# Kernel optimization log

Hardware: AMD Instinct MI355X
Metric: run time of the kernel (lower is better)

## Reference

```python
import jax, jax.numpy as jnp
import numpy as np
from functools import partial

THRESH = 0.6      # objectness sigmoid threshold (forward arg `thresh`)
CASE = 416.0      # input image size (forward arg `case`)
NMS_THRESH = 0.7  # nms(boxes, 0.7, mode='inter')
K_PER_SCALE = 512 # fixed candidate cap per scale (jit-safe stand-in for nonzero())
NEG = -1e9


def _decode_scale(out, t, anchors):
    """out: [N, 3*(5+nc), H, W] -> (boxes [K,9], valid [K]) top-K by objectness."""
    N, C, H, W = out.shape
    v = out.transpose(0, 2, 3, 1).reshape(N, H, W, 3, -1)  # [N,H,W,3,5+nc]
    f = v.dtype
    obj = jax.nn.sigmoid(v[..., 0])                        # cfd = sigmoid(vecs[:,0])
    gy = jnp.arange(H, dtype=f).reshape(1, H, 1, 1)        # idxs[:,1] (row)
    gx = jnp.arange(W, dtype=f).reshape(1, 1, W, 1)        # idxs[:,2] (col)
    gn = jnp.arange(N, dtype=f).reshape(N, 1, 1, 1)
    cx = (gx + v[..., 1]) * t / CASE
    cy = (gy + v[..., 2]) * t / CASE
    w = anchors[:, 0] * jnp.exp(v[..., 3]) / CASE          # anchors[a,0], a = last axis
    h = anchors[:, 1] * jnp.exp(v[..., 4]) / CASE
    cls = jnp.argmax(v[..., 5:], axis=-1).astype(f)
    parts = jnp.broadcast_arrays(gn, cx, cy, w, h, obj, cls, gy + 0 * cx, gx + 0 * cx)
    boxes = jnp.stack(parts, axis=-1).reshape(-1, 9)       # [N*H*W*3, 9]
    mask = (obj > THRESH).reshape(-1)
    score = jnp.where(mask, obj.reshape(-1), NEG)
    k = min(K_PER_SCALE, score.shape[0])
    top_s, top_i = jax.lax.top_k(score, k)
    boxes_k = jnp.take(boxes, top_i, axis=0)
    valid_k = top_s > NEG / 2
    if k < K_PER_SCALE:  # pad to fixed K
        pad = K_PER_SCALE - k
        boxes_k = jnp.concatenate([boxes_k, jnp.zeros((pad, 9), f)], 0)
        valid_k = jnp.concatenate([valid_k, jnp.zeros((pad,), bool)], 0)
    return boxes_k, valid_k


def _nms_inter(boxes, valid):
    """Greedy NMS, iou mode 'inter' = inter_area / min(area_i, area_j)."""
    score = jnp.where(valid, boxes[:, 5], NEG)
    order = jnp.argsort(-score)
    boxes = jnp.take(boxes, order, axis=0)
    valid = jnp.take(valid, order)
    cx, cy, w, h = boxes[:, 1], boxes[:, 2], boxes[:, 3], boxes[:, 4]
    x1, y1, x2, y2 = cx - w / 2, cy - h / 2, cx + w / 2, cy + h / 2
    area = jnp.maximum(x2 - x1, 0) * jnp.maximum(y2 - y1, 0)
    ix = jnp.maximum(0.0, jnp.minimum(x2[:, None], x2[None]) - jnp.maximum(x1[:, None], x1[None]))
    iy = jnp.maximum(0.0, jnp.minimum(y2[:, None], y2[None]) - jnp.maximum(y1[:, None], y1[None]))
    inter = ix * iy
    iou = inter / jnp.maximum(jnp.minimum(area[:, None], area[None]), 1e-9)
    M = boxes.shape[0]
    idx = jnp.arange(M)

    def body(i, keep):
        sup = (iou[i] > NMS_THRESH) & keep[i] & (idx > i)
        return keep & ~sup

    keep = jax.lax.fori_loop(0, M, body, valid)
    return boxes * keep[:, None].astype(boxes.dtype)  # suppressed rows zeroed


def reference(out13, out26, out52, anchors13, anchors26, anchors52):
    b13, v13 = _decode_scale(out13, 32.0, anchors13)
    b26, v26 = _decode_scale(out26, 16.0, anchors26)
    b52, v52 = _decode_scale(out52, 8.0, anchors52)
    boxes = jnp.concatenate([b13, b26, b52], axis=0)   # [3K, 9]
    valid = jnp.concatenate([v13, v26, v52], axis=0)
    return _nms_inter(boxes, valid)


def setup_inputs() -> dict:
    key = jax.random.key(0)
    k = jax.random.split(key, 6)
    N, NC = 32, 80
    C = 3 * (5 + NC)
    return {
        "out13": jax.random.normal(k[0], (N, C, 13, 13), jnp.float32),
        "out26": jax.random.normal(k[1], (N, C, 26, 26), jnp.float32),
        "out52": jax.random.normal(k[2], (N, C, 52, 52), jnp.float32),
        "anchors13": jnp.array([[116, 90], [156, 198], [373, 326]], jnp.float32),
        "anchors26": jnp.array([[30, 61], [62, 45], [59, 119]], jnp.float32),
        "anchors52": jnp.array([[10, 13], [16, 30], [33, 23]], jnp.float32),
    }
```

## Files before the change

### kernel.cpp

```cpp
#include <hip/hip_runtime.h>
#include <stdint.h>

#define KPS 512
#define NBOX 1536
#define NBINS 1024

#define S13 16224
#define S26 64896
#define S52 259584
#define TOTCELL 340704

__device__ __forceinline__ uint32_t f2u(float x){ union{float f;uint32_t u;}v; v.f=x; return v.u; }
__device__ __forceinline__ float u2f(uint32_t x){ union{float f;uint32_t u;}v; v.u=x; return v.f; }

__device__ __forceinline__ int binOf(float s){
    int b = (int)((s - 0.6f) * 2560.0f);
    if (b < 0) b = 0;
    if (b > NBINS-1) b = NBINS-1;
    return b;
}

__global__ void k_score(const float* __restrict__ o13, const float* __restrict__ o26,
                        const float* __restrict__ o52, unsigned* __restrict__ scr){
    int id = blockIdx.x*256 + threadIdx.x;
    if (id >= TOTCELL) return;
    int idl, H;
    const float* src;
    if (id < S13)            { idl=id;            H=13; src=o13; }
    else if (id < S13+S26)   { idl=id-S13;        H=26; src=o26; }
    else                     { idl=id-(S13+S26);  H=52; src=o52; }
    int HW = H*H;
    int p  = idl / HW;
    int hw = idl - p*HW;
    int n  = p / 3;
    int a  = p - n*3;
    float x = src[(size_t)(n*255 + a*85)*HW + hw];
    float s = (float)(1.0 / (1.0 + exp(-(double)x)));
    scr[id] = (s > 0.6f) ? f2u(s) : 0u;
}

template<int H, int SCALE, int OFF, int LEN>
__device__ __forceinline__ void select_impl(const unsigned* __restrict__ scr,
        unsigned long long* __restrict__ sel, int* __restrict__ cnt,
        int* histL, unsigned long long* un, int* sB, int* scA, int* scS){
    constexpr int HW = H*H;
    constexpr int N4 = LEN/4;
    int t = threadIdx.x;
    histL[t] = 0;
    if (t == 0){ *scA = 0; *scS = 0; }
    __syncthreads();
    const uint4* v4 = reinterpret_cast<const uint4*>(scr + OFF);
    for (int i = t; i < N4; i += 1024){
        uint4 u = v4[i];
        if (u.x) atomicAdd(&histL[binOf(u2f(u.x))], 1);
        if (u.y) atomicAdd(&histL[binOf(u2f(u.y))], 1);
        if (u.z) atomicAdd(&histL[binOf(u2f(u.z))], 1);
        if (u.w) atomicAdd(&histL[binOf(u2f(u.w))], 1);
    }
    __syncthreads();
    int h = histL[t];
    for (int d = 1; d < NBINS; d <<= 1){
        int v = (t + d < NBINS) ? histL[t + d] : 0;
        __syncthreads();
        histL[t] += v;
        __syncthreads();
    }
    int total = histL[0];
    int Aab = (t < NBINS-1) ? histL[t+1] : 0;
    if (t == 0 && total < KPS) *sB = -1;
    if (Aab < KPS && Aab + h >= KPS) *sB = t;
    __syncthreads();
    int B = *sB;
    for (int i = t; i < N4; i += 1024){
        uint4 u = v4[i];
        #pragma unroll
        for (int c = 0; c < 4; c++){
            unsigned sb = (c==0)?u.x:(c==1)?u.y:(c==2)?u.z:u.w;
            if (!sb) continue;
            int bin = binOf(u2f(sb));
            if (bin < B) continue;
            int idx = i*4 + c;
            int p  = idx / HW;
            int hw = idx - p*HW;
            int n  = p / 3;
            int a  = p - n*3;
            int cidx = (n*HW + hw)*3 + a;
            unsigned long long key = ((unsigned long long)sb << 20)
                | ((unsigned long long)(2-SCALE) << 18)
                | (unsigned long long)(262143 - cidx);
            if (bin > B){
                int pos = atomicAdd(scA, 1);
                un[pos] = key;
            } else {
                int pos = atomicAdd(scS, 1);
                if (pos < 1024) un[512 + pos] = key;
            }
        }
    }
    __syncthreads();
    int cA = *scA;
    int cSk = *scS; if (cSk > 1024) cSk = 1024;
    int need = KPS - cA; if (need < 0) need = 0;
    int m = (need < cSk) ? need : cSk;
    int Nsel = cA + m;
    int E = cA + cSk;
    for (int e = t; e < E; e += 1024){
        unsigned long long k = (e < cA) ? un[e] : un[512 + e - cA];
        int rank = 0;
        for (int q = 0; q < cA; q++)  rank += (un[q] > k) ? 1 : 0;
        for (int q = 0; q < cSk; q++) rank += (un[512 + q] > k) ? 1 : 0;
        if (rank < Nsel) sel[SCALE*KPS + rank] = k;
    }
    if (t < KPS && t >= Nsel) sel[SCALE*KPS + t] = 0ull;
    if (t == 0) cnt[SCALE] = Nsel;
}

__global__ void __launch_bounds__(1024) k_select(const unsigned* __restrict__ scr,
                        unsigned long long* __restrict__ sel, int* __restrict__ cnt){
    __shared__ int histL[NBINS];
    __shared__ unsigned long long un[1536];
    __shared__ int sB, scA, scS;
    int s = blockIdx.x;
    if (s == 0)      select_impl<13,0,0,        S13>(scr, sel, cnt, histL, un, &sB, &scA, &scS);
    else if (s == 1) select_impl<26,1,S13,      S26>(scr, sel, cnt, histL, un, &sB, &scA, &scS);
    else             select_impl<52,2,S13+S26,  S52>(scr, sel, cnt, histL, un, &sB, &scA, &scS);
}

__global__ void k_decode_merge(const float* __restrict__ o13, const float* __restrict__ o26,
                         const float* __restrict__ o52,
                         const float* __restrict__ a13, const float* __restrict__ a26,
                         const float* __restrict__ a52,
                         const unsigned long long* __restrict__ sel, const int* __restrict__ cnt,
                         float* __restrict__ sboxes, unsigned long long* __restrict__ vwords){
    __shared__ unsigned long long sk[NBOX];
    int t = threadIdx.x;
    for (int r = t; r < NBOX; r += 256) sk[r] = sel[r];
    __syncthreads();
    int wv = t >> 6, lane = t & 63;
    int b = blockIdx.x*4 + wv;
    unsigned long long key = sk[b];
    int pc = 0;
    for (int q = lane; q < NBOX; q += 64){
        unsigned long long kq = sk[q];
        pc += (kq > key || (kq == key && q < b)) ? 1 : 0;
    }
    #pragma unroll
    for (int off = 32; off; off >>= 1) pc += __shfl_xor(pc, off);
    int rank = pc;
    float* row = sboxes + rank*12;
    if ((key >> 20) == 0ull){
        if (lane < 9) row[lane] = 0.f;
    } else {
        int scale = 2 - (int)((key >> 18) & 3ull);
        int cidx  = 262143 - (int)(key & 0x3FFFFull);
        uint32_t sbits = (uint32_t)(key >> 20);
        const float* src; const float* anch; int H; float tt;
        if (scale == 0){ src=o13; anch=a13; H=13; tt=32.f; }
        else if (scale == 1){ src=o26; anch=a26; H=26; tt=16.f; }
        else { src=o52; anch=a52; H=52; tt=8.f; }
        int HW = H*H;
        int a  = cidx % 3;
        int hw = (cidx/3) % HW;
        int n  = cidx / (3*HW);
        int hh = hw / H;
        int ww = hw - hh*H;
        const float* cellbase = src + (size_t)(n*255 + a*85)*HW + hw;
        float bv = cellbase[(size_t)(5 + lane)*HW];
        int bi = lane;
        if (lane < 16){
            float v2 = cellbase[(size_t)(69 + lane)*HW];
            if (v2 > bv){ bv = v2; bi = 64 + lane; }
        }
        #pragma unroll
        for (int off=32; off; off>>=1){
            float vo = __shfl_xor(bv, off);
            int io = __shfl_xor(bi, off);
            if (vo > bv || (vo == bv && io < bi)){ bv = vo; bi = io; }
        }
        if (lane == 0){
            float v1 = cellbase[(size_t)1*HW];
            float v2 = cellbase[(size_t)2*HW];
            float v3 = cellbase[(size_t)3*HW];
            float v4 = cellbase[(size_t)4*HW];
            float cx = ((float)ww + v1) * tt / 416.0f;
            float cy = ((float)hh + v2) * tt / 416.0f;
            float e3 = (float)exp((double)v3);
            float e4 = (float)exp((double)v4);
            float bw = anch[a*2+0] * e3 / 416.0f;
            float bh = anch[a*2+1] * e4 / 416.0f;
            row[0] = (float)n;  row[1] = cx; row[2] = cy; row[3] = bw; row[4] = bh;
            row[5] = u2f(sbits); row[6] = (float)bi; row[7] = (float)hh; row[8] = (float)ww;
        }
    }
    if (blockIdx.x == 0 && t < 24){
        int nv = cnt[0] + cnt[1] + cnt[2];
        int rem = nv - t*64;
        vwords[t] = rem >= 64 ? ~0ull : (rem <= 0 ? 0ull : ((1ull << rem) - 1ull));
    }
}

__global__ void k_masks(const float* __restrict__ sboxes, unsigned* __restrict__ Tcol,
                        unsigned long long* __restrict__ diagR){
    int i = blockIdx.x;
    int lane = threadIdx.x;
    int gi = i >> 6;
    float cxi = sboxes[i*12+1], cyi = sboxes[i*12+2], wi = sboxes[i*12+3], hi = sboxes[i*12+4];
    float x1i = cxi - wi/2.0f, y1i = cyi - hi/2.0f, x2i = cxi + wi/2.0f, y2i = cyi + hi/2.0f;
    float ari = fmaxf(x2i-x1i, 0.f) * fmaxf(y2i-y1i, 0.f);
    unsigned colbits = 0u;
    for (int c=0; c<24; c++){
        int j = c*64 + lane;
        float cxj = sboxes[j*12+1], cyj = sboxes[j*12+2], wj = sboxes[j*12+3], hj = sboxes[j*12+4];
        float x1j = cxj - wj/2.0f, y1j = cyj - hj/2.0f, x2j = cxj + wj/2.0f, y2j = cyj + hj/2.0f;
        float arj = fmaxf(x2j-x1j, 0.f) * fmaxf(y2j-y1j, 0.f);
        float ix = fmaxf(0.f, fminf(x2i, x2j) - fmaxf(x1i, x1j));
        float iy = fmaxf(0.f, fminf(y2i, y2j) - fmaxf(y1i, y1j));
        float inter = ix * iy;
        float iou = inter / fmaxf(fminf(ari, arj), 1e-9f);
        bool sb = (iou > 0.7f) && (j > i);
        colbits |= sb ? (1u << c) : 0u;
    }
    Tcol[(size_t)i*64 + lane] = colbits;
    unsigned long long rowbits = __ballot(((colbits >> gi) & 1u) != 0u);
    if (lane == 0) diagR[i] = rowbits;
}

__device__ __forceinline__ unsigned long long readlane64(unsigned long long v, int i){
    unsigned lo = (unsigned)__builtin_amdgcn_readlane((int)(unsigned)v, i);
    unsigned hi = (unsigned)__builtin_amdgcn_readlane((int)(unsigned)(v >> 32), i);
    return ((unsigned long long)hi << 32) | (unsigned long long)lo;
}

__global__ void k_nms_out(const float* __restrict__ sboxes, const unsigned long long* __restrict__ vwords,
                          const unsigned long long* __restrict__ diagR, const unsigned* __restrict__ Tcol,
                          float* __restrict__ out){
    __shared__ unsigned long long keepw[24];
    __shared__ unsigned partial[2][4][64];
    int t = threadIdx.x;
    int wv = t >> 6, lane = t & 63;
    unsigned SS = 0u;
    unsigned long long rowR = diagR[lane];
    unsigned long long vcur = vwords[0];
    unsigned rows[16];
    {
        const unsigned* b0 = Tcol + (size_t)(wv*16)*64 + lane;
        #pragma unroll
        for (int i=0;i<16;i++) rows[i] = b0[i*64];
    }
    for (int g = 0; g < 24; g++){
        unsigned long long Rnext = (g < 23) ? diagR[(g+1)*64 + lane] : 0ull;
        unsigned long long vnext = (g < 23) ? vwords[g+1] : 0ull;
        bool live = (((vcur >> lane) & 1ull) != 0ull) && (((SS >> g) & 1u) == 0u);
        unsigned long long pend = __ballot(live);
        unsigned long long Z = __ballot(live && ((rowR & pend) != 0ull));
        unsigned long long kept = pend;
        unsigned long long iter = Z;
        while (iter){
            int i = __ffsll((long long)iter) - 1;
            iter &= iter - 1ull;
            if ((kept >> i) & 1ull){
                unsigned long long sup = readlane64(rowR, i);
                kept &= ~sup;
                iter &= ~sup;
            }
        }
        if (t == 0) keepw[g] = kept;
        unsigned kbits = (unsigned)((kept >> (wv*16)) & 0xFFFFull);
        unsigned acc = 0u;
        #pragma unroll
        for (int i=0;i<16;i++) acc |= (0u - ((kbits >> i) & 1u)) & rows[i];
        if (g < 23){
            const unsigned* nb = Tcol + (size_t)((g+1)*64 + wv*16)*64 + lane;
            #pragma unroll
            for (int i=0;i<16;i++) rows[i] = nb[i*64];
        }
        partial[g & 1][wv][lane] = acc;
        __syncthreads();
        SS |= partial[g & 1][0][lane] | partial[g & 1][1][lane]
            | partial[g & 1][2][lane] | partial[g & 1][3][lane];
        rowR = Rnext; vcur = vnext;
    }
    for (int e=t; e<NBOX*9; e+=256){
        int r = e / 9;
        int c = e - r*9;
        bool kp = ((keepw[r >> 6] >> (r & 63)) & 1ull) != 0ull;
        out[e] = kp ? sboxes[r*12 + c] : 0.f;
    }
}

extern "C" void kernel_launch(void* const* d_in, const int* in_sizes, int n_in,
                              void* d_out, int out_size, void* d_ws, size_t ws_size,
                              hipStream_t stream){
    const float* o13 = (const float*)d_in[0];
    const float* o26 = (const float*)d_in[1];
    const float* o52 = (const float*)d_in[2];
    const float* a13 = (const float*)d_in[3];
    const float* a26 = (const float*)d_in[4];
    const float* a52 = (const float*)d_in[5];
    char* ws = (char*)d_ws;
    unsigned* scr             = (unsigned*)(ws);
    unsigned* Tcol            = (unsigned*)(ws);
    int* cnt                  = (int*)(ws + 1362816);
    unsigned long long* sel   = (unsigned long long*)(ws + 1362944);
    float* sboxes             = (float*)(ws + 1375232);
    unsigned long long* vw    = (unsigned long long*)(ws + 1448960);
    unsigned long long* diagR = (unsigned long long*)(ws + 1449216);
    float* out = (float*)d_out;

    k_score       <<<(TOTCELL + 255)/256, 256, 0, stream>>>(o13, o26, o52, scr);
    k_select      <<<3, 1024, 0, stream>>>(scr, sel, cnt);
    k_decode_merge<<<NBOX/4, 256, 0, stream>>>(o13, o26, o52, a13, a26, a52, sel, cnt, sboxes, vw);
    k_masks       <<<NBOX, 64, 0, stream>>>(sboxes, Tcol, diagR);
    k_nms_out     <<<1, 256, 0, stream>>>(sboxes, vw, diagR, Tcol, out);
}
```

Measured before the change: 246.6 us.

## Split per-scale top-K selection into grid-wide histogram, cutoff, classify, finalize kernels

The old selection ran in a single 3-block kernel, so one 1024-thread block scanned about 260K scores for the 52 scale. That work now goes to the whole GPU: k_score builds per-scale histograms with global atomics, a small kernel finds the cutoff bin, a grid-wide classify kernel scatters candidates into above and stash buffers, and a 3-block finalize kernel ranks them. This trades a serial bottleneck for three extra kernel launches and contended global atomics on histogram bins and counters.

After: 248.6 us. About the same (+0.8%).

```diff
diff --git a/kernel.cpp b/kernel.cpp
--- a/kernel.cpp
+++ b/kernel.cpp
@@ -20,15 +20,22 @@
     return b;
 }
 
+__global__ void k_init(int* hist, int* cnt){
+    int id = blockIdx.x*256 + threadIdx.x;
+    if (id < 3*NBINS) hist[id] = 0;
+    if (id < 32) cnt[id] = 0;
+}
+
 __global__ void k_score(const float* __restrict__ o13, const float* __restrict__ o26,
-                        const float* __restrict__ o52, unsigned* __restrict__ scr){
+                        const float* __restrict__ o52,
+                        unsigned* __restrict__ scr, int* __restrict__ hist){
     int id = blockIdx.x*256 + threadIdx.x;
     if (id >= TOTCELL) return;
-    int idl, H;
+    int scale, idl, H;
     const float* src;
-    if (id < S13)            { idl=id;            H=13; src=o13; }
-    else if (id < S13+S26)   { idl=id-S13;        H=26; src=o26; }
-    else                     { idl=id-(S13+S26);  H=52; src=o52; }
+    if (id < S13)            { scale=0; idl=id;            H=13; src=o13; }
+    else if (id < S13+S26)   { scale=1; idl=id-S13;        H=26; src=o26; }
+    else                     { scale=2; idl=id-(S13+S26);  H=52; src=o52; }
     int HW = H*H;
     int p  = idl / HW;
     int hw = idl - p*HW;
@@ -36,94 +43,94 @@
     int a  = p - n*3;
     float x = src[(size_t)(n*255 + a*85)*HW + hw];
     float s = (float)(1.0 / (1.0 + exp(-(double)x)));
-    scr[id] = (s > 0.6f) ? f2u(s) : 0u;
-}
-
-template<int H, int SCALE, int OFF, int LEN>
-__device__ __forceinline__ void select_impl(const unsigned* __restrict__ scr,
-        unsigned long long* __restrict__ sel, int* __restrict__ cnt,
-        int* histL, unsigned long long* un, int* sB, int* scA, int* scS){
-    constexpr int HW = H*H;
-    constexpr int N4 = LEN/4;
-    int t = threadIdx.x;
-    histL[t] = 0;
-    if (t == 0){ *scA = 0; *scS = 0; }
-    __syncthreads();
-    const uint4* v4 = reinterpret_cast<const uint4*>(scr + OFF);
-    for (int i = t; i < N4; i += 1024){
-        uint4 u = v4[i];
-        if (u.x) atomicAdd(&histL[binOf(u2f(u.x))], 1);
-        if (u.y) atomicAdd(&histL[binOf(u2f(u.y))], 1);
-        if (u.z) atomicAdd(&histL[binOf(u2f(u.z))], 1);
-        if (u.w) atomicAdd(&histL[binOf(u2f(u.w))], 1);
-    }
-    __syncthreads();
-    int h = histL[t];
-    for (int d = 1; d < NBINS; d <<= 1){
-        int v = (t + d < NBINS) ? histL[t + d] : 0;
+    if (s > 0.6f){
+        scr[id] = f2u(s);
+        atomicAdd(&hist[scale*NBINS + binOf(s)], 1);
+    } else {
+        scr[id] = 0u;
+    }
+}
+
+__global__ void __launch_bounds__(1024) k_cutoff(const int* __restrict__ hist, int* __restrict__ cnt){
+    int s = blockIdx.x, t = threadIdx.x;
+    __shared__ int suf[NBINS];
+    int h = hist[s*NBINS + t];
+    suf[t] = h; __syncthreads();
+    for (int d=1; d<NBINS; d<<=1){
+        int v = (t+d < NBINS) ? suf[t+d] : 0;
         __syncthreads();
-        histL[t] += v;
+        suf[t] += v;
         __syncthreads();
     }
-    int total = histL[0];
-    int Aab = (t < NBINS-1) ? histL[t+1] : 0;
-    if (t == 0 && total < KPS) *sB = -1;
-    if (Aab < KPS && Aab + h >= KPS) *sB = t;
-    __syncthreads();
-    int B = *sB;
-    for (int i = t; i < N4; i += 1024){
-        uint4 u = v4[i];
-        #pragma unroll
-        for (int c = 0; c < 4; c++){
-            unsigned sb = (c==0)?u.x:(c==1)?u.y:(c==2)?u.z:u.w;
-            if (!sb) continue;
-            int bin = binOf(u2f(sb));
-            if (bin < B) continue;
-            int idx = i*4 + c;
-            int p  = idx / HW;
-            int hw = idx - p*HW;
-            int n  = p / 3;
-            int a  = p - n*3;
-            int cidx = (n*HW + hw)*3 + a;
-            unsigned long long key = ((unsigned long long)sb << 20)
-                | ((unsigned long long)(2-SCALE) << 18)
-                | (unsigned long long)(262143 - cidx);
-            if (bin > B){
-                int pos = atomicAdd(scA, 1);
-                un[pos] = key;
-            } else {
-                int pos = atomicAdd(scS, 1);
-                if (pos < 1024) un[512 + pos] = key;
-            }
-        }
-    }
-    __syncthreads();
-    int cA = *scA;
-    int cSk = *scS; if (cSk > 1024) cSk = 1024;
+    int total = suf[0];
+    int A = (t < NBINS-1) ? suf[t+1] : 0;
+    if (t == 0 && total < KPS) cnt[9+s] = -1;
+    if (A < KPS && A + h >= KPS) cnt[9+s] = t;
+}
+
+__global__ void k_classify(const unsigned* __restrict__ scr, int* __restrict__ cnt,
+                           unsigned long long* __restrict__ above, unsigned long long* __restrict__ stash){
+    int tid = blockIdx.x*256 + threadIdx.x;
+    if (tid >= TOTCELL/4) return;
+    const uint4* v4 = reinterpret_cast<const uint4*>(scr);
+    uint4 u = v4[tid];
+    if (!(u.x | u.y | u.z | u.w)) return;
+    int id0 = tid*4;
+    int scale, off, H;
+    if (id0 < S13)           { scale=0; off=0;       H=13; }
+    else if (id0 < S13+S26)  { scale=1; off=S13;     H=26; }
+    else                     { scale=2; off=S13+S26; H=52; }
+    int HW = H*H;
+    int B = cnt[9+scale];
+    #pragma unroll
+    for (int c = 0; c < 4; c++){
+        unsigned sb = (c==0)?u.x:(c==1)?u.y:(c==2)?u.z:u.w;
+        if (!sb) continue;
+        int bin = binOf(u2f(sb));
+        if (bin < B) continue;
+        int idx = id0 + c - off;
+        int p  = idx / HW;
+        int hw = idx - p*HW;
+        int n  = p / 3;
+        int a  = p - n*3;
+        int cidx = (n*HW + hw)*3 + a;
+        unsigned long long key = ((unsigned long long)sb << 20)
+            | ((unsigned long long)(2-scale) << 18)
+            | (unsigned long long)(262143 - cidx);
+        if (bin > B){
+            int pos = atomicAdd(&cnt[3+scale], 1);
+            if (pos < KPS) above[scale*KPS + pos] = key;
+        } else {
+            int pos = atomicAdd(&cnt[6+scale], 1);
+            if (pos < 1024) stash[scale*1024 + pos] = key;
+        }
+    }
+}
+
+__global__ void __launch_bounds__(1024) k_finalize(int* __restrict__ cnt,
+                           const unsigned long long* __restrict__ above,
+                           const unsigned long long* __restrict__ stash,
+                           unsigned long long* __restrict__ sel){
+    int s = blockIdx.x, t = threadIdx.x;
+    __shared__ unsigned long long un[1536];
+    int cA = cnt[3+s];
+    int cSk = cnt[6+s]; if (cSk > 1024) cSk = 1024;
     int need = KPS - cA; if (need < 0) need = 0;
     int m = (need < cSk) ? need : cSk;
     int Nsel = cA + m;
+    if (t < cA)  un[t] = above[s*KPS + t];
+    if (t < cSk) un[512 + t] = stash[s*1024 + t];
+    __syncthreads();
     int E = cA + cSk;
     for (int e = t; e < E; e += 1024){
         unsigned long long k = (e < cA) ? un[e] : un[512 + e - cA];
         int rank = 0;
         for (int q = 0; q < cA; q++)  rank += (un[q] > k) ? 1 : 0;
         for (int q = 0; q < cSk; q++) rank += (un[512 + q] > k) ? 1 : 0;
-        if (rank < Nsel) sel[SCALE*KPS + rank] = k;
-    }
-    if (t < KPS && t >= Nsel) sel[SCALE*KPS + t] = 0ull;
-    if (t == 0) cnt[SCALE] = Nsel;
-}
-
-__global__ void __launch_bounds__(1024) k_select(const unsigned* __restrict__ scr,
-                        unsigned long long* __restrict__ sel, int* __restrict__ cnt){
-    __shared__ int histL[NBINS];
-    __shared__ unsigned long long un[1536];
-    __shared__ int sB, scA, scS;
-    int s = blockIdx.x;
-    if (s == 0)      select_impl<13,0,0,        S13>(scr, sel, cnt, histL, un, &sB, &scA, &scS);
-    else if (s == 1) select_impl<26,1,S13,      S26>(scr, sel, cnt, histL, un, &sB, &scA, &scS);
-    else             select_impl<52,2,S13+S26,  S52>(scr, sel, cnt, histL, un, &sB, &scA, &scS);
+        if (rank < Nsel) sel[s*KPS + rank] = k;
+    }
+    if (t < KPS && t >= Nsel) sel[s*KPS + t] = 0ull;
+    if (t == 0) cnt[s] = Nsel;
 }
 
 __global__ void k_decode_merge(const float* __restrict__ o13, const float* __restrict__ o26,
@@ -300,15 +307,21 @@
     char* ws = (char*)d_ws;
     unsigned* scr             = (unsigned*)(ws);
     unsigned* Tcol            = (unsigned*)(ws);
-    int* cnt                  = (int*)(ws + 1362816);
-    unsigned long long* sel   = (unsigned long long*)(ws + 1362944);
-    float* sboxes             = (float*)(ws + 1375232);
-    unsigned long long* vw    = (unsigned long long*)(ws + 1448960);
-    unsigned long long* diagR = (unsigned long long*)(ws + 1449216);
+    int* hist                 = (int*)(ws + 1362816);
+    int* cnt                  = (int*)(ws + 1375104);
+    unsigned long long* above = (unsigned long long*)(ws + 1375232);
+    unsigned long long* sel   = (unsigned long long*)(ws + 1387520);
+    unsigned long long* stash = (unsigned long long*)(ws + 1399808);
+    float* sboxes             = (float*)(ws + 1424384);
+    unsigned long long* vw    = (unsigned long long*)(ws + 1498112);
+    unsigned long long* diagR = (unsigned long long*)(ws + 1498368);
     float* out = (float*)d_out;
 
-    k_score       <<<(TOTCELL + 255)/256, 256, 0, stream>>>(o13, o26, o52, scr);
-    k_select      <<<3, 1024, 0, stream>>>(scr, sel, cnt);
+    k_init        <<<12, 256, 0, stream>>>(hist, cnt);
+    k_score       <<<(TOTCELL + 255)/256, 256, 0, stream>>>(o13, o26, o52, scr, hist);
+    k_cutoff      <<<3, NBINS, 0, stream>>>(hist, cnt);
+    k_classify    <<<(TOTCELL/4 + 255)/256, 256, 0, stream>>>(scr, cnt, above, stash);
+    k_finalize    <<<3, 1024, 0, stream>>>(cnt, above, stash, sel);
     k_decode_merge<<<NBOX/4, 256, 0, stream>>>(o13, o26, o52, a13, a26, a52, sel, cnt, sboxes, vw);
     k_masks       <<<NBOX, 64, 0, stream>>>(sboxes, Tcol, diagR);
     k_nms_out     <<<1, 256, 0, stream>>>(sboxes, vw, diagR, Tcol, out);
```
